# Kernel tuning notes

Measured on AMD Instinct MI355X. Metric: run time of the kernel, lower is better.

## Reference

```python
import jax, jax.numpy as jnp
import numpy as np


def setup_inputs() -> dict:
    key = jax.random.key(0)
    ks = jax.random.split(key, 7)
    b, c, t, h, w = 4, 128, 16, 64, 64
    c8 = c // 8
    return {
        "x": jax.random.normal(ks[0], (b, c, t, h, w), dtype=jnp.float32),
        "q_w": jax.random.normal(ks[1], (c8, c), dtype=jnp.float32) * 0.05,
        "q_b": jax.random.normal(ks[2], (c8,), dtype=jnp.float32) * 0.05,
        "k_w": jax.random.normal(ks[3], (c8, c), dtype=jnp.float32) * 0.05,
        "k_b": jax.random.normal(ks[4], (c8,), dtype=jnp.float32) * 0.05,
        "v_w": jax.random.normal(ks[5], (c, c), dtype=jnp.float32) * 0.05,
        "v_b": jax.random.normal(ks[6], (c,), dtype=jnp.float32) * 0.05,
        "gamma": jnp.zeros((1,), dtype=jnp.float32),
    }


def reference(x, q_w, q_b, k_w, k_b, v_w, v_b, gamma):
    # x: [b, c, t, h, w]. 1x1x1 Conv3d == per-position channel matmul.
    # Project directly into the [b, h, w, t, ch] layout the attention uses.
    q = jnp.einsum('bcthw,oc->bhwto', x, q_w) + q_b   # [b,h,w,t,c/8]
    k = jnp.einsum('bcthw,oc->bhwto', x, k_w) + k_b   # [b,h,w,t,c/8]
    v = jnp.einsum('bcthw,oc->bhwto', x, v_w) + v_b   # [b,h,w,t,c]
    # Temporal attention batched over (b,h,w): scores [b,h,w,t_q,t_k]
    scores = jnp.einsum('bhwio,bhwjo->bhwij', q, k)
    attn = jax.nn.softmax(scores, axis=-1)            # softmax over keys (dim=2 in torch [bhw,t,t])
    out = jnp.einsum('bhwij,bhwjo->bhwio', attn, v)   # [b,h,w,t,c]
    out = jnp.transpose(out, (0, 4, 3, 1, 2))         # -> [b,c,t,h,w]
    return gamma * out + x
```

## Files before the change

### kernel.cpp

```cpp
#include <hip/hip_runtime.h>


#define C_  128
#define T_  16
#define H_  64
#define W_  64
#define HW_ (H_*W_)
#define CO_ 160
#define WT_ 32
#define NBLK 512
#define THW (T_*H_*W_)

typedef float  f32x4  __attribute__((ext_vector_type(4)));
typedef short  bf16x4 __attribute__((ext_vector_type(4)));
typedef short  bf16x8 __attribute__((ext_vector_type(8)));

__device__ __forceinline__ unsigned short f2bf(float f) {
    union { float f; unsigned u; } v; v.f = f;
    unsigned r = v.u + 0x7fffu + ((v.u >> 16) & 1u);
    return (unsigned short)(r >> 16);
}
__device__ __forceinline__ float bf2f(unsigned short s) {
    union { unsigned u; float f; } v; v.u = ((unsigned)s) << 16;
    return v.f;
}

__global__ __launch_bounds__(256) void tsa_prepack(
        const float* __restrict__ qw, const float* __restrict__ qb,
        const float* __restrict__ kw, const float* __restrict__ kb,
        const float* __restrict__ vw, const float* __restrict__ vb,
        unsigned short* __restrict__ W2, float* __restrict__ b2) {
    int i = blockIdx.x * 256 + threadIdx.x;
    int o = i >> 7, c = i & 127;
    float v = (o < 16) ? qw[o * C_ + c] : (o < 32) ? kw[(o - 16) * C_ + c]
                                                   : vw[(o - 32) * C_ + c];
    W2[i] = f2bf(v);
    if (i < CO_) b2[i] = (i < 16) ? qb[i] : (i < 32) ? kb[i - 16] : vb[i - 32];
}

#define PS 2184
#define TS 136
#define IDX_X(pos, t, c)   ((pos) * PS + (t) * TS + (c))
#define QOFF 69888
#define QIDX(wv, qk, t, o) (QOFF + (wv) * 640 + (qk) * 320 + (t) * 20 + (o))
#define BIAS_OFF 75008
#define BUF_SH 75328

__global__ __launch_bounds__(512) void tsa_main(
        const float* __restrict__ x, const unsigned short* __restrict__ W2,
        const float* __restrict__ b2, const float* __restrict__ gamma,
        float* __restrict__ y) {

    __shared__ __align__(16) unsigned short buf[BUF_SH];
    float* bias_lds = (float*)&buf[BIAS_OFF];

    int bid  = blockIdx.x;
    int work = (bid & 7) * (NBLK / 8) + (bid >> 3);
    int bh = work >> 1;
    int wt = work & 1;
    int b  = bh >> 6, h = bh & 63;
    int w0 = wt * WT_;

    const size_t base = (size_t)b * C_ * THW + (size_t)h * W_ + w0;
    const float* xb = x + base;
    float*       yb = y + base;

    const int tid = threadIdx.x;
    const int seg = tid & 7;
    const int cs0 = tid >> 3;
    const float g = gamma[0];

    const int wv  = tid >> 6;
    const int lr  = tid & 15;
    const int grp = (tid & 63) >> 4;

    if (tid < CO_) bias_lds[tid] = b2[tid];

    #pragma unroll
    for (int r = 0; r < 2; ++r) {
        const int cs  = cs0 + 64 * r;
        const int loc = cs ^ (seg << 3);
        const float* xcol = xb + (size_t)cs * THW + seg * 4;
        f32x4 xa[8];
        #pragma unroll
        for (int t = 0; t < 8; ++t) xa[t] = *(const f32x4*)(xcol + t * HW_);
        #pragma unroll
        for (int t = 0; t < 8; ++t)
            #pragma unroll
            for (int e = 0; e < 4; ++e)
                buf[IDX_X(seg * 4 + e, t, loc)] = f2bf(xa[t][e]);
        #pragma unroll
        for (int t = 0; t < 8; ++t) xa[t] = *(const f32x4*)(xcol + (t + 8) * HW_);
        #pragma unroll
        for (int t = 0; t < 8; ++t)
            #pragma unroll
            for (int e = 0; e < 4; ++e)
                buf[IDX_X(seg * 4 + e, t + 8, loc)] = f2bf(xa[t][e]);
    }
    __syncthreads();

    const int swz = wv << 3;
    for (int pp = 0; pp < 4; ++pp) {
        const int pos = wv * 4 + pp;

        bf16x8 afrag[4];
        #pragma unroll
        for (int ks = 0; ks < 4; ++ks)
            afrag[ks] = *(const bf16x8*)&buf[IDX_X(pos, lr, (ks * 32 + grp * 8) ^ swz)];

        bf16x4 vreg[8];
        #pragma unroll
        for (int nt = 0; nt < 10; ++nt) {
            f32x4 acc = (f32x4){0.f, 0.f, 0.f, 0.f};
            #pragma unroll
            for (int ks = 0; ks < 4; ++ks) {
                bf16x8 wf = *(const bf16x8*)&W2[(nt * 16 + lr) * C_ + ks * 32 + grp * 8];
                acc = __builtin_amdgcn_mfma_f32_16x16x32_bf16(afrag[ks], wf, acc, 0, 0, 0);
            }
            float bv = bias_lds[nt * 16 + lr];
            if (nt < 2) {
                #pragma unroll
                for (int rr = 0; rr < 4; ++rr)
                    buf[QIDX(wv, nt, grp * 4 + rr, lr)] = f2bf(acc[rr] + bv);
            } else {
                bf16x4 pk;
                #pragma unroll
                for (int rr = 0; rr < 4; ++rr) pk[rr] = (short)f2bf(acc[rr] + bv);
                vreg[nt - 2] = pk;
            }
        }

        bf16x4 kf = *(const bf16x4*)&buf[QIDX(wv, 1, lr, grp * 4)];
        bf16x4 qf = *(const bf16x4*)&buf[QIDX(wv, 0, lr, grp * 4)];
        f32x4 s = (f32x4){0.f, 0.f, 0.f, 0.f};
        s = __builtin_amdgcn_mfma_f32_16x16x16bf16_1k(kf, qf, s, 0, 0, 0);
        float mx = fmaxf(fmaxf(s[0], s[1]), fmaxf(s[2], s[3]));
        mx = fmaxf(mx, __shfl_xor(mx, 16));
        mx = fmaxf(mx, __shfl_xor(mx, 32));
        float e0 = __expf(s[0] - mx), e1 = __expf(s[1] - mx);
        float e2 = __expf(s[2] - mx), e3 = __expf(s[3] - mx);
        float sm = e0 + e1 + e2 + e3;
        sm += __shfl_xor(sm, 16);
        sm += __shfl_xor(sm, 32);
        float inv = 1.0f / sm;
        bf16x4 pf;
        pf[0] = (short)f2bf(e0 * inv); pf[1] = (short)f2bf(e1 * inv);
        pf[2] = (short)f2bf(e2 * inv); pf[3] = (short)f2bf(e3 * inv);

        #pragma unroll
        for (int ct = 0; ct < 8; ++ct) {
            f32x4 z = (f32x4){0.f, 0.f, 0.f, 0.f};
            z = __builtin_amdgcn_mfma_f32_16x16x16bf16_1k(vreg[ct], pf, z, 0, 0, 0);
            bf16x4 ob;
            #pragma unroll
            for (int rr = 0; rr < 4; ++rr) ob[rr] = (short)f2bf(z[rr]);
            *(bf16x4*)&buf[IDX_X(pos, lr, (ct * 16 + grp * 4) ^ swz)] = ob;
        }
    }
    __syncthreads();

    #pragma unroll
    for (int r = 0; r < 2; ++r) {
        const int cs  = cs0 + 64 * r;
        const int loc = cs ^ (seg << 3);
        const float* xrow = xb + (size_t)cs * THW + seg * 4;
        float*       yrow = yb + (size_t)cs * THW + seg * 4;
        #pragma unroll
        for (int half = 0; half < 2; ++half) {
            const int t0 = half * 8;
            f32x4 xa[8];
            #pragma unroll
            for (int t = 0; t < 8; ++t) xa[t] = *(const f32x4*)(xrow + (t0 + t) * HW_);
            #pragma unroll
            for (int t = 0; t < 8; ++t) {
                f32x4 rv;
                #pragma unroll
                for (int e = 0; e < 4; ++e)
                    rv[e] = fmaf(g, bf2f(buf[IDX_X(seg * 4 + e, t0 + t, loc)]), xa[t][e]);
                *(f32x4*)(yrow + (t0 + t) * HW_) = rv;
            }
        }
    }
}

extern "C" void kernel_launch(void* const* d_in, const int* in_sizes, int n_in,
                              void* d_out, int out_size, void* d_ws, size_t ws_size,
                              hipStream_t stream) {
    const float* x  = (const float*)d_in[0];
    const float* qw = (const float*)d_in[1];
    const float* qb = (const float*)d_in[2];
    const float* kw = (const float*)d_in[3];
    const float* kb = (const float*)d_in[4];
    const float* vw = (const float*)d_in[5];
    const float* vb = (const float*)d_in[6];
    const float* gm = (const float*)d_in[7];
    float* y = (float*)d_out;

    unsigned short* W2 = (unsigned short*)d_ws;
    float* b2 = (float*)((char*)d_ws + CO_ * C_ * sizeof(unsigned short));

    tsa_prepack<<<80, 256, 0, stream>>>(qw, qb, kw, kb, vw, vb, W2, b2);
    tsa_main<<<NBLK, 512, 0, stream>>>(x, W2, b2, gm, y);
}
```

Measured before the change: 99.44 us.

## Process two positions per pass, pre-swizzle weights, prefetch residual x

Repacks the projection weights into an MFMA-fragment-ordered layout so each lane reads one contiguous 16-byte chunk. The projection loop now handles two spatial positions per pass, so each weight fragment load feeds two MFMAs. The first residual chunk of x is also prefetched before the final barrier to overlap global latency. The cost is more live registers (two accumulator sets, two vreg arrays, plus the prefetch), which may reduce occupancy. Two unroll pragmas are removed.

```diff
diff --git a/kernel.cpp b/kernel.cpp
--- a/kernel.cpp
+++ b/kernel.cpp
@@ -29,12 +29,16 @@
         const float* __restrict__ qw, const float* __restrict__ qb,
         const float* __restrict__ kw, const float* __restrict__ kb,
         const float* __restrict__ vw, const float* __restrict__ vb,
-        unsigned short* __restrict__ W2, float* __restrict__ b2) {
+        unsigned short* __restrict__ W2, float* __restrict__ b2,
+        unsigned short* __restrict__ W3) {
     int i = blockIdx.x * 256 + threadIdx.x;
     int o = i >> 7, c = i & 127;
     float v = (o < 16) ? qw[o * C_ + c] : (o < 32) ? kw[(o - 16) * C_ + c]
                                                    : vw[(o - 32) * C_ + c];
-    W2[i] = f2bf(v);
+    unsigned short u = f2bf(v);
+    W2[i] = u;
+    int nt = o >> 4, lr = o & 15, ks = c >> 5, gp = (c >> 3) & 3, j = c & 7;
+    W3[(((nt * 4 + ks) * 64) + gp * 16 + lr) * 8 + j] = u;
     if (i < CO_) b2[i] = (i < 16) ? qb[i] : (i < 32) ? kb[i - 16] : vb[i - 32];
 }
 
@@ -47,7 +51,7 @@
 #define BUF_SH 75328
 
 __global__ __launch_bounds__(512) void tsa_main(
-        const float* __restrict__ x, const unsigned short* __restrict__ W2,
+        const float* __restrict__ x, const unsigned short* __restrict__ W3,
         const float* __restrict__ b2, const float* __restrict__ gamma,
         float* __restrict__ y) {
 
@@ -65,10 +69,11 @@
     const float* xb = x + base;
     float*       yb = y + base;
 
-    const int tid = threadIdx.x;
-    const int seg = tid & 7;
-    const int cs0 = tid >> 3;
-    const float g = gamma[0];
+    const int tid  = threadIdx.x;
+    const int lane = tid & 63;
+    const int seg  = tid & 7;
+    const int cs0  = tid >> 3;
+    const float g  = gamma[0];
 
     const int wv  = tid >> 6;
     const int lr  = tid & 15;
@@ -76,7 +81,6 @@
 
     if (tid < CO_) bias_lds[tid] = b2[tid];
 
-    #pragma unroll
     for (int r = 0; r < 2; ++r) {
         const int cs  = cs0 + 64 * r;
         const int loc = cs ^ (seg << 3);
@@ -100,66 +104,95 @@
     __syncthreads();
 
     const int swz = wv << 3;
-    for (int pp = 0; pp < 4; ++pp) {
-        const int pos = wv * 4 + pp;
-
-        bf16x8 afrag[4];
-        #pragma unroll
-        for (int ks = 0; ks < 4; ++ks)
-            afrag[ks] = *(const bf16x8*)&buf[IDX_X(pos, lr, (ks * 32 + grp * 8) ^ swz)];
-
-        bf16x4 vreg[8];
+    for (int pr = 0; pr < 2; ++pr) {
+        const int posA = wv * 4 + pr * 2;
+        const int posB = posA + 1;
+
+        bf16x8 afA[4], afB[4];
+        #pragma unroll
+        for (int ks = 0; ks < 4; ++ks) {
+            afA[ks] = *(const bf16x8*)&buf[IDX_X(posA, lr, (ks * 32 + grp * 8) ^ swz)];
+            afB[ks] = *(const bf16x8*)&buf[IDX_X(posB, lr, (ks * 32 + grp * 8) ^ swz)];
+        }
+
+        bf16x4 vreg[2][8];
+        bf16x4 qkB[2];
         #pragma unroll
         for (int nt = 0; nt < 10; ++nt) {
-            f32x4 acc = (f32x4){0.f, 0.f, 0.f, 0.f};
+            f32x4 acc0 = (f32x4){0.f, 0.f, 0.f, 0.f};
+            f32x4 acc1 = (f32x4){0.f, 0.f, 0.f, 0.f};
             #pragma unroll
             for (int ks = 0; ks < 4; ++ks) {
-                bf16x8 wf = *(const bf16x8*)&W2[(nt * 16 + lr) * C_ + ks * 32 + grp * 8];
-                acc = __builtin_amdgcn_mfma_f32_16x16x32_bf16(afrag[ks], wf, acc, 0, 0, 0);
+                bf16x8 wf = *(const bf16x8*)&W3[(((nt * 4 + ks) * 64) + lane) * 8];
+                acc0 = __builtin_amdgcn_mfma_f32_16x16x32_bf16(afA[ks], wf, acc0, 0, 0, 0);
+                acc1 = __builtin_amdgcn_mfma_f32_16x16x32_bf16(afB[ks], wf, acc1, 0, 0, 0);
             }
             float bv = bias_lds[nt * 16 + lr];
             if (nt < 2) {
                 #pragma unroll
                 for (int rr = 0; rr < 4; ++rr)
-                    buf[QIDX(wv, nt, grp * 4 + rr, lr)] = f2bf(acc[rr] + bv);
+                    buf[QIDX(wv, nt, grp * 4 + rr, lr)] = f2bf(acc0[rr] + bv);
+                bf16x4 pk;
+                #pragma unroll
+                for (int rr = 0; rr < 4; ++rr) pk[rr] = (short)f2bf(acc1[rr] + bv);
+                qkB[nt] = pk;
             } else {
-                bf16x4 pk;
-                #pragma unroll
-                for (int rr = 0; rr < 4; ++rr) pk[rr] = (short)f2bf(acc[rr] + bv);
-                vreg[nt - 2] = pk;
-            }
-        }
-
-        bf16x4 kf = *(const bf16x4*)&buf[QIDX(wv, 1, lr, grp * 4)];
-        bf16x4 qf = *(const bf16x4*)&buf[QIDX(wv, 0, lr, grp * 4)];
-        f32x4 s = (f32x4){0.f, 0.f, 0.f, 0.f};
-        s = __builtin_amdgcn_mfma_f32_16x16x16bf16_1k(kf, qf, s, 0, 0, 0);
-        float mx = fmaxf(fmaxf(s[0], s[1]), fmaxf(s[2], s[3]));
-        mx = fmaxf(mx, __shfl_xor(mx, 16));
-        mx = fmaxf(mx, __shfl_xor(mx, 32));
-        float e0 = __expf(s[0] - mx), e1 = __expf(s[1] - mx);
-        float e2 = __expf(s[2] - mx), e3 = __expf(s[3] - mx);
-        float sm = e0 + e1 + e2 + e3;
-        sm += __shfl_xor(sm, 16);
-        sm += __shfl_xor(sm, 32);
-        float inv = 1.0f / sm;
-        bf16x4 pf;
-        pf[0] = (short)f2bf(e0 * inv); pf[1] = (short)f2bf(e1 * inv);
-        pf[2] = (short)f2bf(e2 * inv); pf[3] = (short)f2bf(e3 * inv);
-
-        #pragma unroll
-        for (int ct = 0; ct < 8; ++ct) {
-            f32x4 z = (f32x4){0.f, 0.f, 0.f, 0.f};
-            z = __builtin_amdgcn_mfma_f32_16x16x16bf16_1k(vreg[ct], pf, z, 0, 0, 0);
-            bf16x4 ob;
-            #pragma unroll
-            for (int rr = 0; rr < 4; ++rr) ob[rr] = (short)f2bf(z[rr]);
-            *(bf16x4*)&buf[IDX_X(pos, lr, (ct * 16 + grp * 4) ^ swz)] = ob;
+                bf16x4 pA, pB;
+                #pragma unroll
+                for (int rr = 0; rr < 4; ++rr) {
+                    pA[rr] = (short)f2bf(acc0[rr] + bv);
+                    pB[rr] = (short)f2bf(acc1[rr] + bv);
+                }
+                vreg[0][nt - 2] = pA;
+                vreg[1][nt - 2] = pB;
+            }
+        }
+
+        #pragma unroll
+        for (int p = 0; p < 2; ++p) {
+            const int pos = p ? posB : posA;
+            if (p) {
+                #pragma unroll
+                for (int rr = 0; rr < 4; ++rr) {
+                    buf[QIDX(wv, 0, grp * 4 + rr, lr)] = (unsigned short)qkB[0][rr];
+                    buf[QIDX(wv, 1, grp * 4 + rr, lr)] = (unsigned short)qkB[1][rr];
+                }
+            }
+            bf16x4 kf = *(const bf16x4*)&buf[QIDX(wv, 1, lr, grp * 4)];
+            bf16x4 qf = *(const bf16x4*)&buf[QIDX(wv, 0, lr, grp * 4)];
+            f32x4 s = (f32x4){0.f, 0.f, 0.f, 0.f};
+            s = __builtin_amdgcn_mfma_f32_16x16x16bf16_1k(kf, qf, s, 0, 0, 0);
+            float mx = fmaxf(fmaxf(s[0], s[1]), fmaxf(s[2], s[3]));
+            mx = fmaxf(mx, __shfl_xor(mx, 16));
+            mx = fmaxf(mx, __shfl_xor(mx, 32));
+            float e0 = __expf(s[0] - mx), e1 = __expf(s[1] - mx);
+            float e2 = __expf(s[2] - mx), e3 = __expf(s[3] - mx);
+            float sm = e0 + e1 + e2 + e3;
+            sm += __shfl_xor(sm, 16);
+            sm += __shfl_xor(sm, 32);
+            float inv = 1.0f / sm;
+            bf16x4 pf;
+            pf[0] = (short)f2bf(e0 * inv); pf[1] = (short)f2bf(e1 * inv);
+            pf[2] = (short)f2bf(e2 * inv); pf[3] = (short)f2bf(e3 * inv);
+            #pragma unroll
+            for (int ct = 0; ct < 8; ++ct) {
+                f32x4 z = (f32x4){0.f, 0.f, 0.f, 0.f};
+                z = __builtin_amdgcn_mfma_f32_16x16x16bf16_1k(vreg[p][ct], pf, z, 0, 0, 0);
+                bf16x4 ob;
+                #pragma unroll
+                for (int rr = 0; rr < 4; ++rr) ob[rr] = (short)f2bf(z[rr]);
+                *(bf16x4*)&buf[IDX_X(pos, lr, (ct * 16 + grp * 4) ^ swz)] = ob;
+            }
         }
     }
+
+    const float* xrow0 = xb + (size_t)cs0 * THW + seg * 4;
+    f32x4 pre[8];
+    #pragma unroll
+    for (int t = 0; t < 8; ++t) pre[t] = *(const f32x4*)(xrow0 + t * HW_);
+
     __syncthreads();
 
-    #pragma unroll
     for (int r = 0; r < 2; ++r) {
         const int cs  = cs0 + 64 * r;
         const int loc = cs ^ (seg << 3);
@@ -169,8 +202,13 @@
         for (int half = 0; half < 2; ++half) {
             const int t0 = half * 8;
             f32x4 xa[8];
-            #pragma unroll
-            for (int t = 0; t < 8; ++t) xa[t] = *(const f32x4*)(xrow + (t0 + t) * HW_);
+            if (r == 0 && half == 0) {
+                #pragma unroll
+                for (int t = 0; t < 8; ++t) xa[t] = pre[t];
+            } else {
+                #pragma unroll
+                for (int t = 0; t < 8; ++t) xa[t] = *(const f32x4*)(xrow + (t0 + t) * HW_);
+            }
             #pragma unroll
             for (int t = 0; t < 8; ++t) {
                 f32x4 rv;
@@ -197,8 +235,9 @@
     float* y = (float*)d_out;
 
     unsigned short* W2 = (unsigned short*)d_ws;
-    float* b2 = (float*)((char*)d_ws + CO_ * C_ * sizeof(unsigned short));
-
-    tsa_prepack<<<80, 256, 0, stream>>>(qw, qb, kw, kb, vw, vb, W2, b2);
-    tsa_main<<<NBLK, 512, 0, stream>>>(x, W2, b2, gm, y);
-}
+    float*          b2 = (float*)((char*)d_ws + 40960);
+    unsigned short* W3 = (unsigned short*)((char*)d_ws + 41600);
+
+    tsa_prepack<<<80, 256, 0, stream>>>(qw, qb, kw, kb, vw, vb, W2, b2, W3);
+    tsa_main<<<NBLK, 512, 0, stream>>>(x, W3, b2, gm, y);
+}
```

Result: faster. 84.14 us (median of 2 runs) (-15.4%).
